# Kernel tuning notes

Measured on AMD Instinct MI355X. Metric: run time of the kernel, lower is better.

## Reference

```python
import jax, jax.numpy as jnp
import numpy as np
import math

CW = 10
T_S = 2.0


def _K(t0):
    t = t0 - CW // 2
    if t < 0:
        return -0.5 * math.exp(t / (T_S / 2.0))
    return math.exp(-t / T_S)

K_VALS = np.array([_K(k) for k in range(CW)], dtype=np.float32)          # synaptic kernel
KS_VALS = np.array([math.exp(-k / T_S) for k in range(CW)], dtype=np.float32)  # spike kernel


def swish(v):
    # original Swish: x * sigmoid(10*x)
    return v * jax.nn.sigmoid(10.0 * v)


def act_fun(v):
    # smooth surrogate spike activation: sigmoid(10*(mem - 0.5)), thresh=0.5
    return jax.nn.sigmoid(10.0 * (v - 0.5))


def setup_inputs() -> dict:
    key = jax.random.key(0)
    k1, k2, k3, k4 = jax.random.split(key, 4)
    B, T = 4096, 50
    x = jax.random.uniform(k1, (B, T, 620), dtype=jnp.float32)
    W1 = jax.random.normal(k2, (200, 620), dtype=jnp.float32) / np.sqrt(620.0)
    W2 = jax.random.normal(k3, (100, 200), dtype=jnp.float32) / np.sqrt(200.0)
    W3 = jax.random.normal(k4, (11, 100), dtype=jnp.float32) / np.sqrt(100.0)
    return {"x": x, "W1": W1, "W2": W2, "W3": W3}


def reference(x, W1, W2, W3):
    B, T, _ = x.shape
    kv = jnp.asarray(K_VALS)
    ks_tail = jnp.asarray(KS_VALS[1:])   # k=1..9; k=0 spike term is always 0 (buffer not yet written)
    kv_tail = jnp.asarray(K_VALS[1:])    # k=1..9 for layer-input history

    # h1 is purely feedforward in time -> precompute, then causal conv with K over CW window.
    h1 = swish(jnp.einsum('btd,nd->btn', x, W1))            # [B, T, 200]
    h1_pad = jnp.pad(h1, ((0, 0), (CW - 1, 0), (0, 0)))
    syn2 = sum(kv[k] * h1_pad[:, CW - 1 - k: CW - 1 - k + T] for k in range(CW))  # [B, T, 200]

    def shift(hist, new):
        # hist[:, j] holds value at time t-1-j; prepend current value
        return jnp.concatenate([new[:, None], hist[:, :-1]], axis=1)

    def step(carry, syn2_t):
        sl2_h, h2_h, sl3_h, h3_h, sl4_h, acc = carry
        # layer 2
        mem2 = syn2_t - jnp.einsum('k,bkn->bn', ks_tail, sl2_h)
        s2 = act_fun(mem2)
        sl2 = s2 * mem2
        h2 = swish(s2 @ W2.T)                                # [B, 100]
        # layer 3
        mem3 = kv[0] * h2 + jnp.einsum('k,bkn->bn', kv_tail, h2_h) \
               - jnp.einsum('k,bkn->bn', ks_tail, sl3_h)
        s3 = act_fun(mem3)
        sl3 = s3 * mem3
        h3 = swish(s3 @ W3.T)                                # [B, 11]
        # layer 4 (output)
        mem4 = kv[0] * h3 + jnp.einsum('k,bkn->bn', kv_tail, h3_h) \
               - jnp.einsum('k,bkn->bn', ks_tail, sl4_h)
        s4 = act_fun(mem4)
        sl4 = s4 * mem4
        carry = (shift(sl2_h, sl2), shift(h2_h, h2), shift(sl3_h, sl3),
                 shift(h3_h, h3), shift(sl4_h, sl4), acc + s4)
        return carry, None

    z = lambda n: jnp.zeros((B, CW - 1, n), dtype=x.dtype)
    carry0 = (z(200), z(100), z(100), z(11), z(11), jnp.zeros((B, 11), dtype=x.dtype))
    carry, _ = jax.lax.scan(step, carry0, jnp.swapaxes(syn2, 0, 1))
    h4_sumspike = carry[-1]
    return h4_sumspike / 50.0
```

## Files before the change

### kernel.cpp

```cpp
#include <hip/hip_runtime.h>
#include <math.h>

#define T_STEPS 50
#define D_IN    620
#define N1      200
#define N2      100
#define N3      11
#define BATCH   4096

typedef short bf16x8 __attribute__((ext_vector_type(8)));
typedef float f32x4  __attribute__((ext_vector_type(4)));

__device__ __constant__ float KV[10] = {
    -0.0033689735f, -0.0091578194f, -0.0248935342f, -0.0676676416f, -0.1839397206f,
     1.0f,           0.6065306597f,  0.3678794412f,  0.2231301601f,  0.1353352832f };

#define RHO    0.60653066f
#define RHO5   0.0820849986f
#define RHO10  0.0067379470f
#define KV0    (-0.0033689735f)
#define C1     (-0.0091578194f)
#define C2     (-0.0248935342f)
#define C3     (-0.0676676416f)
#define C4     (-0.1839397206f)

__device__ __forceinline__ float sigm10(float x) { return 1.0f / (1.0f + __expf(-10.0f * x)); }
__device__ __forceinline__ float swishf(float v) { return v / (1.0f + __expf(-10.0f * v)); }

__device__ __forceinline__ void split2(float x, unsigned short& hi, unsigned short& lo) {
    unsigned u = __float_as_uint(x);
    hi = (unsigned short)(u >> 16);
    float rem = x - __uint_as_float(u & 0xFFFF0000u);
    lo = (unsigned short)(__float_as_uint(rem) >> 16);
}

__global__ void prep_w1(const float* __restrict__ W1, unsigned short* __restrict__ W1pre) {
    int i = blockIdx.x * 256 + threadIdx.x;
    if (i >= 266240) return;
    int kk = i & 31;
    int t1 = i >> 5;
    int n  = t1 % 208;
    int t2 = t1 / 208;
    int p  = t2 & 1;
    int kt = t2 >> 1;
    int k  = kt * 32 + kk;
    float w = (n < N1 && k < D_IN) ? W1[n * D_IN + k] : 0.0f;
    unsigned short hi, lo; split2(w, hi, lo);
    int gsw = (kk >> 3) ^ ((n >> 1) & 3);
    int idx = kt * 13312 + p * 6656 + n * 32 + gsw * 8 + (kk & 7);
    W1pre[idx] = p ? lo : hi;
}

__global__ void prep_w2(const float* __restrict__ W2, unsigned short* __restrict__ W2pre2) {
    int i = blockIdx.x * 256 + threadIdx.x;
    if (i >= 57344) return;
    int e  = i & 7;
    int r  = i >> 3;
    int l  = r & 63;
    int r2 = r >> 6;
    int p  = r2 & 1;
    int r3 = r2 >> 1;
    int ks = r3 % 7;
    int wv = r3 / 7;
    int n  = wv * 16 + (l & 15);
    int k  = ks * 32 + (l >> 4) * 8 + e;
    float v = (n < N2 && k < N1) ? W2[n * N1 + k] : 0.0f;
    unsigned short hi, lo; split2(v, hi, lo);
    W2pre2[i] = p ? lo : hi;
}

__global__ __launch_bounds__(512, 4) void gemm1_mfma(const float* __restrict__ x,
                                                     const unsigned short* __restrict__ W1pre,
                                                     float* __restrict__ h1) {
    __shared__ unsigned short Bs[3][13312];

    const int tid = threadIdx.x;
    const int w   = tid >> 6;
    const int l   = tid & 63;
    const int j   = l >> 4;
    const int r16 = l & 15;
    const long row0 = (long)blockIdx.x * 128;
    const float* arow = x + (row0 + w * 16 + r16) * D_IN;

    f32x4 acc[13];
#pragma unroll
    for (int nt = 0; nt < 13; ++nt) acc[nt] = (f32x4){0.f, 0.f, 0.f, 0.f};

    auto stageB = [&](int kt, int bb) {
        const unsigned short* src = W1pre + kt * 13312;
        unsigned short* dst = &Bs[bb][0];
#pragma unroll
        for (int it = 0; it < 3; ++it) {
            int ch = it * 512 + tid;
            __builtin_amdgcn_global_load_lds(
                (const __attribute__((address_space(1))) unsigned int*)(src + ch * 8),
                (__attribute__((address_space(3))) unsigned int*)(dst + ch * 8), 16, 0, 0);
        }
        if (tid < 128) {
            int ch = 1536 + tid;
            __builtin_amdgcn_global_load_lds(
                (const __attribute__((address_space(1))) unsigned int*)(src + ch * 8),
                (__attribute__((address_space(3))) unsigned int*)(dst + ch * 8), 16, 0, 0);
        }
    };

    auto loadA = [&](int kt, float* av) {
        const float* p = arow + kt * 32 + j * 8;
        const float4 u0 = *(const float4*)p;
        const float4 u1 = *(const float4*)(p + 4);
        av[0] = u0.x; av[1] = u0.y; av[2] = u0.z; av[3] = u0.w;
        av[4] = u1.x; av[5] = u1.y; av[6] = u1.z; av[7] = u1.w;
    };
    auto loadAtail = [&](float* av) {
        if (j == 0) {
            const float4 u0 = *(const float4*)(arow + 608);
            const float4 u1 = *(const float4*)(arow + 612);
            av[0] = u0.x; av[1] = u0.y; av[2] = u0.z; av[3] = u0.w;
            av[4] = u1.x; av[5] = u1.y; av[6] = u1.z; av[7] = u1.w;
        } else if (j == 1) {
            const float4 u0 = *(const float4*)(arow + 616);
            av[0] = u0.x; av[1] = u0.y; av[2] = u0.z; av[3] = u0.w;
            av[4] = 0.f; av[5] = 0.f; av[6] = 0.f; av[7] = 0.f;
        } else {
#pragma unroll
            for (int e = 0; e < 8; ++e) av[e] = 0.f;
        }
    };

    float av[2][8];
    stageB(0, 0);
    stageB(1, 1);
    loadA(0, av[0]);
    loadA(1, av[1]);
    asm volatile("s_waitcnt vmcnt(7)" ::: "memory");
    asm volatile("s_barrier" ::: "memory");

#pragma unroll 1
    for (int kt = 0; kt < 20; ++kt) {
        bf16x8 ah, al;
#pragma unroll
        for (int e = 0; e < 8; ++e) {
            unsigned short hi, lo; split2(av[kt & 1][e], hi, lo);
            ah[e] = (short)hi; al[e] = (short)lo;
        }
        if (kt < 18) {
            if (kt + 2 == 19) loadAtail(av[kt & 1]); else loadA(kt + 2, av[kt & 1]);
            stageB(kt + 2, (kt + 2) % 3);
        }
        const unsigned short* B = &Bs[kt % 3][0];
#pragma unroll
        for (int nt = 0; nt < 13; ++nt) {
            const int n  = nt * 16 + r16;
            const int gs = j ^ ((n >> 1) & 3);
            const bf16x8 bh = *(const bf16x8*)(B + n * 32 + gs * 8);
            const bf16x8 bl = *(const bf16x8*)(B + 6656 + n * 32 + gs * 8);
            acc[nt] = __builtin_amdgcn_mfma_f32_16x16x32_bf16(ah, bh, acc[nt], 0, 0, 0);
            acc[nt] = __builtin_amdgcn_mfma_f32_16x16x32_bf16(ah, bl, acc[nt], 0, 0, 0);
            acc[nt] = __builtin_amdgcn_mfma_f32_16x16x32_bf16(al, bh, acc[nt], 0, 0, 0);
        }
        if (kt < 18) {
            asm volatile("s_waitcnt vmcnt(5)" ::: "memory");
            asm volatile("s_barrier" ::: "memory");
        } else if (kt == 18) {
            asm volatile("s_waitcnt vmcnt(0)" ::: "memory");
            asm volatile("s_barrier" ::: "memory");
        }
    }

#pragma unroll
    for (int nt = 0; nt < 13; ++nt) {
        const int gcol = nt * 16 + r16;
        if (gcol < N1) {
            const long grow0 = row0 + w * 16 + j * 4;
#pragma unroll
            for (int q = 0; q < 4; ++q)
                h1[(grow0 + q) * N1 + gcol] = swishf(acc[nt][q]);
        }
    }
}

__global__ __launch_bounds__(256) void conv_k(float* __restrict__ buf) {
    __shared__ float h1s[T_STEPS * N1];
    const int b = blockIdx.x, tid = threadIdx.x;
    float* p = buf + (size_t)b * (T_STEPS * N1);
    for (int i = tid; i < T_STEPS * N1 / 4; i += 256)
        ((float4*)h1s)[i] = ((const float4*)p)[i];
    __syncthreads();
    for (int i = tid; i < T_STEPS * N1; i += 256) {
        int t = i / N1, n = i - t * N1;
        float s = 0.0f;
#pragma unroll
        for (int k = 0; k < 10; ++k)
            if (k <= t) s = fmaf(KV[k], h1s[(t - k) * N1 + n], s);
        p[i] = s;
    }
}

__global__ __launch_bounds__(512, 2) void snn_scan5(const float* __restrict__ syn2,
                                                    const unsigned short* __restrict__ W2pre2,
                                                    const float* __restrict__ W3,
                                                    float* __restrict__ out) {
    __shared__ __align__(16) unsigned short s2A[8192];
    __shared__ __align__(16) float h2buf[8][132];
    __shared__ __align__(16) float s3buf[8][104];
    __shared__ __align__(16) float W3s[N3 * N2];
    __shared__ __align__(16) float pbuf[8][4][12];

    const int tid = threadIdx.x;
    const int wv  = tid >> 6;
    const int l   = tid & 63;
    const int m16 = l & 15;
    const int j2  = l >> 4;
    const int g   = wv;
    const int c   = l;
    const long b  = (long)blockIdx.x * 8 + g;

    for (int i = tid; i < N3 * N2; i += 512) W3s[i] = W3[i];
    for (int i = tid; i < 8192; i += 512) s2A[i] = 0;

    bf16x8 bh[7], bl[7];
    {
        const unsigned short* wp = W2pre2 + wv * 7168 + l * 8;
#pragma unroll
        for (int ks = 0; ks < 7; ++ks) {
            bh[ks] = *(const bf16x8*)(wp + ks * 1024);
            bl[ks] = *(const bf16x8*)(wp + ks * 1024 + 512);
        }
    }

    const int NL2 = (c < 8)  ? 4 : 3;
    const int NL3 = (c < 36) ? 2 : 1;
    const int o4  = c % 11;
    const int p4  = c / 11;
    const int kbeg = (p4 == 0) ? 0 : (4 + 24 * p4);
    const int nf4  = (p4 == 0) ? 7 : 6;

    float sl2h[10][4] = {}; float Ssl2[4] = {};
    float h2h[10][2]  = {}; float Dd3[2]  = {};
    float sl3h[10][2] = {}; float Ssl3[2] = {};
    float h3h[10]     = {}; float Dd4 = 0.f;
    float sl4h[10]    = {}; float Ssl4 = 0.f;
    float accum       = 0.0f;

    const float* syn2b = syn2 + b * (T_STEPS * N1);
    float syn_nxt[4];
#pragma unroll
    for (int jj = 0; jj < 4; ++jj) syn_nxt[jj] = (jj < NL2) ? syn2b[c + 64 * jj] : 0.0f;

    __syncthreads();

#pragma unroll 1
    for (int tb = 0; tb < T_STEPS; tb += 10) {
#pragma unroll
        for (int u = 0; u < 10; ++u) {
            const int t   = tb + u;
            const int um1 = (u + 9) % 10;
            const int um2 = (u + 8) % 10;
            const int um3 = (u + 7) % 10;
            const int um4 = (u + 6) % 10;
            const int um5 = (u + 5) % 10;

            float syn_cur[4];
#pragma unroll
            for (int jj = 0; jj < 4; ++jj) syn_cur[jj] = syn_nxt[jj];
            if (t + 1 < T_STEPS) {
#pragma unroll
                for (int jj = 0; jj < 4; ++jj)
                    if (jj < NL2) syn_nxt[jj] = syn2b[(t + 1) * N1 + c + 64 * jj];
            }

#pragma unroll
            for (int jj = 0; jj < 4; ++jj) {
                if (jj < NL2) {
                    const int n = c + 64 * jj;
                    const float slp = sl2h[um1][jj];
                    const float slo = sl2h[u][jj];
                    Ssl2[jj] = RHO * (Ssl2[jj] + slp) - RHO10 * slo;
                    const float mem2 = syn_cur[jj] - Ssl2[jj];
                    const float s2   = sigm10(mem2 - 0.5f);
                    sl2h[u][jj] = s2 * mem2;
                    unsigned short hi, lo; split2(s2, hi, lo);
                    const int off = g * 256 + (((n >> 3) ^ (g & 7)) * 8) + (n & 7);
                    s2A[off]        = hi;
                    s2A[4096 + off] = lo;
                }
            }
            __syncthreads();

            {
                f32x4 a0 = (f32x4){0.f, 0.f, 0.f, 0.f};
                f32x4 a1 = (f32x4){0.f, 0.f, 0.f, 0.f};
                const int swz = m16 & 7;
#pragma unroll
                for (int ks = 0; ks < 7; ++ks) {
                    const int gr = (4 * ks + j2) ^ swz;
                    const bf16x8 ahv = *(const bf16x8*)&s2A[m16 * 256 + gr * 8];
                    const bf16x8 alv = *(const bf16x8*)&s2A[4096 + m16 * 256 + gr * 8];
                    if (ks & 1) {
                        a1 = __builtin_amdgcn_mfma_f32_16x16x32_bf16(ahv, bh[ks], a1, 0, 0, 0);
                        a1 = __builtin_amdgcn_mfma_f32_16x16x32_bf16(alv, bh[ks], a1, 0, 0, 0);
                        a1 = __builtin_amdgcn_mfma_f32_16x16x32_bf16(ahv, bl[ks], a1, 0, 0, 0);
                    } else {
                        a0 = __builtin_amdgcn_mfma_f32_16x16x32_bf16(ahv, bh[ks], a0, 0, 0, 0);
                        a0 = __builtin_amdgcn_mfma_f32_16x16x32_bf16(alv, bh[ks], a0, 0, 0, 0);
                        a0 = __builtin_amdgcn_mfma_f32_16x16x32_bf16(ahv, bl[ks], a0, 0, 0, 0);
                    }
                }
                const f32x4 a = a0 + a1;
                if (j2 < 2) {
#pragma unroll
                    for (int q = 0; q < 4; ++q)
                        h2buf[j2 * 4 + q][wv * 16 + m16] = swishf(a[q]);
                }
            }
            __syncthreads();

#pragma unroll
            for (int jj = 0; jj < 2; ++jj) {
                if (jj < NL3) {
                    const int m = c + 64 * jj;
                    const float hm = h2buf[g][m];
                    float gneg = C1 * h2h[um1][jj];
                    gneg = fmaf(C2, h2h[um2][jj], gneg);
                    gneg = fmaf(C3, h2h[um3][jj], gneg);
                    gneg = fmaf(C4, h2h[um4][jj], gneg);
                    Dd3[jj] = fmaf(RHO, Dd3[jj], h2h[um5][jj]);
                    Dd3[jj] = fmaf(-RHO5, h2h[u][jj], Dd3[jj]);
                    const float slp = sl3h[um1][jj];
                    const float slo = sl3h[u][jj];
                    Ssl3[jj] = RHO * (Ssl3[jj] + slp) - RHO10 * slo;
                    const float mem3 = fmaf(KV0, hm, gneg) + Dd3[jj] - Ssl3[jj];
                    const float s3   = sigm10(mem3 - 0.5f);
                    sl3h[u][jj] = s3 * mem3;
                    h2h[u][jj]  = hm;
                    s3buf[g][m] = s3;
                }
            }
            asm volatile("s_waitcnt lgkmcnt(0)" ::: "memory");
            __builtin_amdgcn_sched_barrier(0);

            if (c < 44) {
                float part = 0.0f;
#pragma unroll
                for (int i = 0; i < 7; ++i) {
                    if (i < nf4) {
                        const float4 sv  = *(const float4*)&s3buf[g][kbeg + 4 * i];
                        const float4 wv4 = *(const float4*)&W3s[o4 * N2 + kbeg + 4 * i];
                        part = fmaf(sv.x, wv4.x, part);
                        part = fmaf(sv.y, wv4.y, part);
                        part = fmaf(sv.z, wv4.z, part);
                        part = fmaf(sv.w, wv4.w, part);
                    }
                }
                pbuf[g][p4][o4] = part;
            }
            asm volatile("s_waitcnt lgkmcnt(0)" ::: "memory");
            __builtin_amdgcn_sched_barrier(0);

            if (c < N3) {
                const float a4 = pbuf[g][0][c] + pbuf[g][1][c] + pbuf[g][2][c] + pbuf[g][3][c];
                const float h3 = swishf(a4);
                float gneg = C1 * h3h[um1];
                gneg = fmaf(C2, h3h[um2], gneg);
                gneg = fmaf(C3, h3h[um3], gneg);
                gneg = fmaf(C4, h3h[um4], gneg);
                Dd4 = fmaf(RHO, Dd4, h3h[um5]);
                Dd4 = fmaf(-RHO5, h3h[u], Dd4);
                const float slp = sl4h[um1];
                const float slo = sl4h[u];
                Ssl4 = RHO * (Ssl4 + slp) - RHO10 * slo;
                const float mem4 = fmaf(KV0, h3, gneg) + Dd4 - Ssl4;
                const float s4   = sigm10(mem4 - 0.5f);
                sl4h[u] = s4 * mem4;
                h3h[u]  = h3;
                accum += s4;
            }
        }
    }

    if (c < N3) out[b * N3 + c] = accum * 0.02f;
}

extern "C" void kernel_launch(void* const* d_in, const int* in_sizes, int n_in,
                              void* d_out, int out_size, void* d_ws, size_t ws_size,
                              hipStream_t stream) {
    const float* x  = (const float*)d_in[0];
    const float* W1 = (const float*)d_in[1];
    const float* W2 = (const float*)d_in[2];
    const float* W3 = (const float*)d_in[3];
    float* out = (float*)d_out;

    float* buf = (float*)d_ws;
    unsigned short* W1pre  = (unsigned short*)(buf + (size_t)BATCH * T_STEPS * N1);
    unsigned short* W2pre2 = W1pre + 266240;

    prep_w1<<<1040, 256, 0, stream>>>(W1, W1pre);
    prep_w2<<<224, 256, 0, stream>>>(W2, W2pre2);
    gemm1_mfma<<<1600, 512, 0, stream>>>(x, W1pre, buf);
    conv_k<<<BATCH, 256, 0, stream>>>(buf);
    snn_scan5<<<BATCH / 8, 512, 0, stream>>>(buf, W2pre2, W3, out);
}
```

Measured before the change: 529.7 us.

## Fuse causal conv into scan kernel and double GEMM1 row tile per wave

Removes the separate conv_k kernel by computing the layer-1 synaptic convolution inside the scan, using a 10-entry register history and a decaying recursion like the other layers. This avoids a full read and write pass over the large h1 buffer plus one launch. GEMM1 now gives each wave two 16-row M tiles, so each B fragment loaded from LDS is reused twice. The price is roughly doubled accumulator registers and a lower occupancy bound (2 instead of 4), plus extra register pressure in the scan kernel.

```diff
diff --git a/kernel.cpp b/kernel.cpp
--- a/kernel.cpp
+++ b/kernel.cpp
@@ -10,10 +10,6 @@
 
 typedef short bf16x8 __attribute__((ext_vector_type(8)));
 typedef float f32x4  __attribute__((ext_vector_type(4)));
-
-__device__ __constant__ float KV[10] = {
-    -0.0033689735f, -0.0091578194f, -0.0248935342f, -0.0676676416f, -0.1839397206f,
-     1.0f,           0.6065306597f,  0.3678794412f,  0.2231301601f,  0.1353352832f };
 
 #define RHO    0.60653066f
 #define RHO5   0.0820849986f
@@ -69,7 +65,7 @@
     W2pre2[i] = p ? lo : hi;
 }
 
-__global__ __launch_bounds__(512, 4) void gemm1_mfma(const float* __restrict__ x,
+__global__ __launch_bounds__(512, 2) void gemm1_mfma(const float* __restrict__ x,
                                                      const unsigned short* __restrict__ W1pre,
                                                      float* __restrict__ h1) {
     __shared__ unsigned short Bs[3][13312];
@@ -79,12 +75,14 @@
     const int l   = tid & 63;
     const int j   = l >> 4;
     const int r16 = l & 15;
-    const long row0 = (long)blockIdx.x * 128;
-    const float* arow = x + (row0 + w * 16 + r16) * D_IN;
-
-    f32x4 acc[13];
-#pragma unroll
-    for (int nt = 0; nt < 13; ++nt) acc[nt] = (f32x4){0.f, 0.f, 0.f, 0.f};
+    const long row0 = (long)blockIdx.x * 256;
+    const float* arow0 = x + (row0 + w * 32 + r16) * D_IN;
+
+    f32x4 acc[2][13];
+#pragma unroll
+    for (int mt = 0; mt < 2; ++mt)
+#pragma unroll
+        for (int nt = 0; nt < 13; ++nt) acc[mt][nt] = (f32x4){0.f, 0.f, 0.f, 0.f};
 
     auto stageB = [&](int kt, int bb) {
         const unsigned short* src = W1pre + kt * 13312;
@@ -104,45 +102,54 @@
         }
     };
 
-    auto loadA = [&](int kt, float* av) {
-        const float* p = arow + kt * 32 + j * 8;
-        const float4 u0 = *(const float4*)p;
-        const float4 u1 = *(const float4*)(p + 4);
-        av[0] = u0.x; av[1] = u0.y; av[2] = u0.z; av[3] = u0.w;
-        av[4] = u1.x; av[5] = u1.y; av[6] = u1.z; av[7] = u1.w;
+    auto loadA = [&](int kt, float (&av)[2][8]) {
+#pragma unroll
+        for (int mt = 0; mt < 2; ++mt) {
+            const float* p = arow0 + mt * 16 * D_IN + kt * 32 + j * 8;
+            const float4 u0 = *(const float4*)p;
+            const float4 u1 = *(const float4*)(p + 4);
+            av[mt][0] = u0.x; av[mt][1] = u0.y; av[mt][2] = u0.z; av[mt][3] = u0.w;
+            av[mt][4] = u1.x; av[mt][5] = u1.y; av[mt][6] = u1.z; av[mt][7] = u1.w;
+        }
     };
-    auto loadAtail = [&](float* av) {
-        if (j == 0) {
-            const float4 u0 = *(const float4*)(arow + 608);
-            const float4 u1 = *(const float4*)(arow + 612);
-            av[0] = u0.x; av[1] = u0.y; av[2] = u0.z; av[3] = u0.w;
-            av[4] = u1.x; av[5] = u1.y; av[6] = u1.z; av[7] = u1.w;
-        } else if (j == 1) {
-            const float4 u0 = *(const float4*)(arow + 616);
-            av[0] = u0.x; av[1] = u0.y; av[2] = u0.z; av[3] = u0.w;
-            av[4] = 0.f; av[5] = 0.f; av[6] = 0.f; av[7] = 0.f;
-        } else {
-#pragma unroll
-            for (int e = 0; e < 8; ++e) av[e] = 0.f;
+    auto loadAtail = [&](float (&av)[2][8]) {
+#pragma unroll
+        for (int mt = 0; mt < 2; ++mt) {
+            const float* ar = arow0 + mt * 16 * D_IN;
+            if (j == 0) {
+                const float4 u0 = *(const float4*)(ar + 608);
+                const float4 u1 = *(const float4*)(ar + 612);
+                av[mt][0] = u0.x; av[mt][1] = u0.y; av[mt][2] = u0.z; av[mt][3] = u0.w;
+                av[mt][4] = u1.x; av[mt][5] = u1.y; av[mt][6] = u1.z; av[mt][7] = u1.w;
+            } else if (j == 1) {
+                const float4 u0 = *(const float4*)(ar + 616);
+                av[mt][0] = u0.x; av[mt][1] = u0.y; av[mt][2] = u0.z; av[mt][3] = u0.w;
+                av[mt][4] = 0.f; av[mt][5] = 0.f; av[mt][6] = 0.f; av[mt][7] = 0.f;
+            } else {
+#pragma unroll
+                for (int e = 0; e < 8; ++e) av[mt][e] = 0.f;
+            }
         }
     };
 
-    float av[2][8];
+    float av[2][2][8];
     stageB(0, 0);
     stageB(1, 1);
     loadA(0, av[0]);
     loadA(1, av[1]);
-    asm volatile("s_waitcnt vmcnt(7)" ::: "memory");
+    asm volatile("s_waitcnt vmcnt(11)" ::: "memory");
     asm volatile("s_barrier" ::: "memory");
 
 #pragma unroll 1
     for (int kt = 0; kt < 20; ++kt) {
-        bf16x8 ah, al;
-#pragma unroll
-        for (int e = 0; e < 8; ++e) {
-            unsigned short hi, lo; split2(av[kt & 1][e], hi, lo);
-            ah[e] = (short)hi; al[e] = (short)lo;
-        }
+        bf16x8 ah[2], al[2];
+#pragma unroll
+        for (int mt = 0; mt < 2; ++mt)
+#pragma unroll
+            for (int e = 0; e < 8; ++e) {
+                unsigned short hi, lo; split2(av[kt & 1][mt][e], hi, lo);
+                ah[mt][e] = (short)hi; al[mt][e] = (short)lo;
+            }
         if (kt < 18) {
             if (kt + 2 == 19) loadAtail(av[kt & 1]); else loadA(kt + 2, av[kt & 1]);
             stageB(kt + 2, (kt + 2) % 3);
@@ -154,12 +161,15 @@
             const int gs = j ^ ((n >> 1) & 3);
             const bf16x8 bh = *(const bf16x8*)(B + n * 32 + gs * 8);
             const bf16x8 bl = *(const bf16x8*)(B + 6656 + n * 32 + gs * 8);
-            acc[nt] = __builtin_amdgcn_mfma_f32_16x16x32_bf16(ah, bh, acc[nt], 0, 0, 0);
-            acc[nt] = __builtin_amdgcn_mfma_f32_16x16x32_bf16(ah, bl, acc[nt], 0, 0, 0);
-            acc[nt] = __builtin_amdgcn_mfma_f32_16x16x32_bf16(al, bh, acc[nt], 0, 0, 0);
+            acc[0][nt] = __builtin_amdgcn_mfma_f32_16x16x32_bf16(ah[0], bh, acc[0][nt], 0, 0, 0);
+            acc[1][nt] = __builtin_amdgcn_mfma_f32_16x16x32_bf16(ah[1], bh, acc[1][nt], 0, 0, 0);
+            acc[0][nt] = __builtin_amdgcn_mfma_f32_16x16x32_bf16(ah[0], bl, acc[0][nt], 0, 0, 0);
+            acc[1][nt] = __builtin_amdgcn_mfma_f32_16x16x32_bf16(ah[1], bl, acc[1][nt], 0, 0, 0);
+            acc[0][nt] = __builtin_amdgcn_mfma_f32_16x16x32_bf16(al[0], bh, acc[0][nt], 0, 0, 0);
+            acc[1][nt] = __builtin_amdgcn_mfma_f32_16x16x32_bf16(al[1], bh, acc[1][nt], 0, 0, 0);
         }
         if (kt < 18) {
-            asm volatile("s_waitcnt vmcnt(5)" ::: "memory");
+            asm volatile("s_waitcnt vmcnt(7)" ::: "memory");
             asm volatile("s_barrier" ::: "memory");
         } else if (kt == 18) {
             asm volatile("s_waitcnt vmcnt(0)" ::: "memory");
@@ -168,35 +178,21 @@
     }
 
 #pragma unroll
-    for (int nt = 0; nt < 13; ++nt) {
-        const int gcol = nt * 16 + r16;
-        if (gcol < N1) {
-            const long grow0 = row0 + w * 16 + j * 4;
-#pragma unroll
-            for (int q = 0; q < 4; ++q)
-                h1[(grow0 + q) * N1 + gcol] = swishf(acc[nt][q]);
+    for (int mt = 0; mt < 2; ++mt) {
+        const long grow0 = row0 + w * 32 + mt * 16 + j * 4;
+#pragma unroll
+        for (int nt = 0; nt < 13; ++nt) {
+            const int gcol = nt * 16 + r16;
+            if (gcol < N1) {
+#pragma unroll
+                for (int q = 0; q < 4; ++q)
+                    h1[(grow0 + q) * N1 + gcol] = swishf(acc[mt][nt][q]);
+            }
         }
     }
 }
 
-__global__ __launch_bounds__(256) void conv_k(float* __restrict__ buf) {
-    __shared__ float h1s[T_STEPS * N1];
-    const int b = blockIdx.x, tid = threadIdx.x;
-    float* p = buf + (size_t)b * (T_STEPS * N1);
-    for (int i = tid; i < T_STEPS * N1 / 4; i += 256)
-        ((float4*)h1s)[i] = ((const float4*)p)[i];
-    __syncthreads();
-    for (int i = tid; i < T_STEPS * N1; i += 256) {
-        int t = i / N1, n = i - t * N1;
-        float s = 0.0f;
-#pragma unroll
-        for (int k = 0; k < 10; ++k)
-            if (k <= t) s = fmaf(KV[k], h1s[(t - k) * N1 + n], s);
-        p[i] = s;
-    }
-}
-
-__global__ __launch_bounds__(512, 2) void snn_scan5(const float* __restrict__ syn2,
+__global__ __launch_bounds__(512, 2) void snn_scan6(const float* __restrict__ h1,
                                                     const unsigned short* __restrict__ W2pre2,
                                                     const float* __restrict__ W3,
                                                     float* __restrict__ out) {
@@ -236,16 +232,17 @@
     const int nf4  = (p4 == 0) ? 7 : 6;
 
     float sl2h[10][4] = {}; float Ssl2[4] = {};
+    float h1h[10][4]  = {}; float Dsyn[4] = {};
     float h2h[10][2]  = {}; float Dd3[2]  = {};
     float sl3h[10][2] = {}; float Ssl3[2] = {};
     float h3h[10]     = {}; float Dd4 = 0.f;
     float sl4h[10]    = {}; float Ssl4 = 0.f;
     float accum       = 0.0f;
 
-    const float* syn2b = syn2 + b * (T_STEPS * N1);
-    float syn_nxt[4];
-#pragma unroll
-    for (int jj = 0; jj < 4; ++jj) syn_nxt[jj] = (jj < NL2) ? syn2b[c + 64 * jj] : 0.0f;
+    const float* h1b = h1 + b * (T_STEPS * N1);
+    float h1_nxt[4];
+#pragma unroll
+    for (int jj = 0; jj < 4; ++jj) h1_nxt[jj] = (jj < NL2) ? h1b[c + 64 * jj] : 0.0f;
 
     __syncthreads();
 
@@ -260,25 +257,32 @@
             const int um4 = (u + 6) % 10;
             const int um5 = (u + 5) % 10;
 
-            float syn_cur[4];
-#pragma unroll
-            for (int jj = 0; jj < 4; ++jj) syn_cur[jj] = syn_nxt[jj];
+            float h1_cur[4];
+#pragma unroll
+            for (int jj = 0; jj < 4; ++jj) h1_cur[jj] = h1_nxt[jj];
             if (t + 1 < T_STEPS) {
 #pragma unroll
                 for (int jj = 0; jj < 4; ++jj)
-                    if (jj < NL2) syn_nxt[jj] = syn2b[(t + 1) * N1 + c + 64 * jj];
+                    if (jj < NL2) h1_nxt[jj] = h1b[(t + 1) * N1 + c + 64 * jj];
             }
 
 #pragma unroll
             for (int jj = 0; jj < 4; ++jj) {
                 if (jj < NL2) {
                     const int n = c + 64 * jj;
-                    const float slp = sl2h[um1][jj];
-                    const float slo = sl2h[u][jj];
-                    Ssl2[jj] = RHO * (Ssl2[jj] + slp) - RHO10 * slo;
-                    const float mem2 = syn_cur[jj] - Ssl2[jj];
+                    const float hm1 = h1_cur[jj];
+                    float gneg = C1 * h1h[um1][jj];
+                    gneg = fmaf(C2, h1h[um2][jj], gneg);
+                    gneg = fmaf(C3, h1h[um3][jj], gneg);
+                    gneg = fmaf(C4, h1h[um4][jj], gneg);
+                    Dsyn[jj] = fmaf(RHO, Dsyn[jj], h1h[um5][jj]);
+                    Dsyn[jj] = fmaf(-RHO5, h1h[u][jj], Dsyn[jj]);
+                    const float syn = fmaf(KV0, hm1, gneg) + Dsyn[jj];
+                    Ssl2[jj] = RHO * (Ssl2[jj] + sl2h[um1][jj]) - RHO10 * sl2h[u][jj];
+                    const float mem2 = syn - Ssl2[jj];
                     const float s2   = sigm10(mem2 - 0.5f);
                     sl2h[u][jj] = s2 * mem2;
+                    h1h[u][jj]  = hm1;
                     unsigned short hi, lo; split2(s2, hi, lo);
                     const int off = g * 256 + (((n >> 3) ^ (g & 7)) * 8) + (n & 7);
                     s2A[off]        = hi;
@@ -326,9 +330,7 @@
                     gneg = fmaf(C4, h2h[um4][jj], gneg);
                     Dd3[jj] = fmaf(RHO, Dd3[jj], h2h[um5][jj]);
                     Dd3[jj] = fmaf(-RHO5, h2h[u][jj], Dd3[jj]);
-                    const float slp = sl3h[um1][jj];
-                    const float slo = sl3h[u][jj];
-                    Ssl3[jj] = RHO * (Ssl3[jj] + slp) - RHO10 * slo;
+                    Ssl3[jj] = RHO * (Ssl3[jj] + sl3h[um1][jj]) - RHO10 * sl3h[u][jj];
                     const float mem3 = fmaf(KV0, hm, gneg) + Dd3[jj] - Ssl3[jj];
                     const float s3   = sigm10(mem3 - 0.5f);
                     sl3h[u][jj] = s3 * mem3;
@@ -366,9 +368,7 @@
                 gneg = fmaf(C4, h3h[um4], gneg);
                 Dd4 = fmaf(RHO, Dd4, h3h[um5]);
                 Dd4 = fmaf(-RHO5, h3h[u], Dd4);
-                const float slp = sl4h[um1];
-                const float slo = sl4h[u];
-                Ssl4 = RHO * (Ssl4 + slp) - RHO10 * slo;
+                Ssl4 = RHO * (Ssl4 + sl4h[um1]) - RHO10 * sl4h[u];
                 const float mem4 = fmaf(KV0, h3, gneg) + Dd4 - Ssl4;
                 const float s4   = sigm10(mem4 - 0.5f);
                 sl4h[u] = s4 * mem4;
@@ -396,7 +396,6 @@
 
     prep_w1<<<1040, 256, 0, stream>>>(W1, W1pre);
     prep_w2<<<224, 256, 0, stream>>>(W2, W2pre2);
-    gemm1_mfma<<<1600, 512, 0, stream>>>(x, W1pre, buf);
-    conv_k<<<BATCH, 256, 0, stream>>>(buf);
-    snn_scan5<<<BATCH / 8, 512, 0, stream>>>(buf, W2pre2, W3, out);
-}
+    gemm1_mfma<<<800, 512, 0, stream>>>(x, W1pre, buf);
+    snn_scan6<<<BATCH / 8, 512, 0, stream>>>(buf, W2pre2, W3, out);
+}
```

Measured after the change: 850.8 us. +60.6%, slower.

## Fuse causal conv into scan kernel using register history of h1

Applied to the files above, without the earlier changes.

Removes the separate conv_k kernel and computes the synaptic convolution of h1 inside the scan. It uses a 10-step register ring buffer plus a recursive decay accumulator, the same scheme already used for layers 3 and 4. This saves one full read-modify-write pass over the 4096x50x200 h1 buffer and one kernel launch. In exchange it adds about 40 history registers per thread, and launch bounds drop from 2 to 1 blocks per SM minimum, which may reduce occupancy.

```diff
diff --git a/kernel.cpp b/kernel.cpp
--- a/kernel.cpp
+++ b/kernel.cpp
@@ -10,10 +10,6 @@
 
 typedef short bf16x8 __attribute__((ext_vector_type(8)));
 typedef float f32x4  __attribute__((ext_vector_type(4)));
-
-__device__ __constant__ float KV[10] = {
-    -0.0033689735f, -0.0091578194f, -0.0248935342f, -0.0676676416f, -0.1839397206f,
-     1.0f,           0.6065306597f,  0.3678794412f,  0.2231301601f,  0.1353352832f };
 
 #define RHO    0.60653066f
 #define RHO5   0.0820849986f
@@ -179,24 +175,7 @@
     }
 }
 
-__global__ __launch_bounds__(256) void conv_k(float* __restrict__ buf) {
-    __shared__ float h1s[T_STEPS * N1];
-    const int b = blockIdx.x, tid = threadIdx.x;
-    float* p = buf + (size_t)b * (T_STEPS * N1);
-    for (int i = tid; i < T_STEPS * N1 / 4; i += 256)
-        ((float4*)h1s)[i] = ((const float4*)p)[i];
-    __syncthreads();
-    for (int i = tid; i < T_STEPS * N1; i += 256) {
-        int t = i / N1, n = i - t * N1;
-        float s = 0.0f;
-#pragma unroll
-        for (int k = 0; k < 10; ++k)
-            if (k <= t) s = fmaf(KV[k], h1s[(t - k) * N1 + n], s);
-        p[i] = s;
-    }
-}
-
-__global__ __launch_bounds__(512, 2) void snn_scan5(const float* __restrict__ syn2,
+__global__ __launch_bounds__(512, 1) void snn_scan6(const float* __restrict__ h1,
                                                     const unsigned short* __restrict__ W2pre2,
                                                     const float* __restrict__ W3,
                                                     float* __restrict__ out) {
@@ -236,16 +215,17 @@
     const int nf4  = (p4 == 0) ? 7 : 6;
 
     float sl2h[10][4] = {}; float Ssl2[4] = {};
+    float h1h[10][4]  = {}; float Dsyn[4] = {};
     float h2h[10][2]  = {}; float Dd3[2]  = {};
     float sl3h[10][2] = {}; float Ssl3[2] = {};
     float h3h[10]     = {}; float Dd4 = 0.f;
     float sl4h[10]    = {}; float Ssl4 = 0.f;
     float accum       = 0.0f;
 
-    const float* syn2b = syn2 + b * (T_STEPS * N1);
-    float syn_nxt[4];
-#pragma unroll
-    for (int jj = 0; jj < 4; ++jj) syn_nxt[jj] = (jj < NL2) ? syn2b[c + 64 * jj] : 0.0f;
+    const float* h1b = h1 + b * (T_STEPS * N1);
+    float h1_nxt[4];
+#pragma unroll
+    for (int jj = 0; jj < 4; ++jj) h1_nxt[jj] = (jj < NL2) ? h1b[c + 64 * jj] : 0.0f;
 
     __syncthreads();
 
@@ -260,25 +240,32 @@
             const int um4 = (u + 6) % 10;
             const int um5 = (u + 5) % 10;
 
-            float syn_cur[4];
-#pragma unroll
-            for (int jj = 0; jj < 4; ++jj) syn_cur[jj] = syn_nxt[jj];
+            float h1_cur[4];
+#pragma unroll
+            for (int jj = 0; jj < 4; ++jj) h1_cur[jj] = h1_nxt[jj];
             if (t + 1 < T_STEPS) {
 #pragma unroll
                 for (int jj = 0; jj < 4; ++jj)
-                    if (jj < NL2) syn_nxt[jj] = syn2b[(t + 1) * N1 + c + 64 * jj];
+                    if (jj < NL2) h1_nxt[jj] = h1b[(t + 1) * N1 + c + 64 * jj];
             }
 
 #pragma unroll
             for (int jj = 0; jj < 4; ++jj) {
                 if (jj < NL2) {
                     const int n = c + 64 * jj;
-                    const float slp = sl2h[um1][jj];
-                    const float slo = sl2h[u][jj];
-                    Ssl2[jj] = RHO * (Ssl2[jj] + slp) - RHO10 * slo;
-                    const float mem2 = syn_cur[jj] - Ssl2[jj];
+                    const float hm1 = h1_cur[jj];
+                    float gneg = C1 * h1h[um1][jj];
+                    gneg = fmaf(C2, h1h[um2][jj], gneg);
+                    gneg = fmaf(C3, h1h[um3][jj], gneg);
+                    gneg = fmaf(C4, h1h[um4][jj], gneg);
+                    Dsyn[jj] = fmaf(RHO, Dsyn[jj], h1h[um5][jj]);
+                    Dsyn[jj] = fmaf(-RHO5, h1h[u][jj], Dsyn[jj]);
+                    const float syn = fmaf(KV0, hm1, gneg) + Dsyn[jj];
+                    Ssl2[jj] = RHO * (Ssl2[jj] + sl2h[um1][jj]) - RHO10 * sl2h[u][jj];
+                    const float mem2 = syn - Ssl2[jj];
                     const float s2   = sigm10(mem2 - 0.5f);
                     sl2h[u][jj] = s2 * mem2;
+                    h1h[u][jj]  = hm1;
                     unsigned short hi, lo; split2(s2, hi, lo);
                     const int off = g * 256 + (((n >> 3) ^ (g & 7)) * 8) + (n & 7);
                     s2A[off]        = hi;
@@ -326,9 +313,7 @@
                     gneg = fmaf(C4, h2h[um4][jj], gneg);
                     Dd3[jj] = fmaf(RHO, Dd3[jj], h2h[um5][jj]);
                     Dd3[jj] = fmaf(-RHO5, h2h[u][jj], Dd3[jj]);
-                    const float slp = sl3h[um1][jj];
-                    const float slo = sl3h[u][jj];
-                    Ssl3[jj] = RHO * (Ssl3[jj] + slp) - RHO10 * slo;
+                    Ssl3[jj] = RHO * (Ssl3[jj] + sl3h[um1][jj]) - RHO10 * sl3h[u][jj];
                     const float mem3 = fmaf(KV0, hm, gneg) + Dd3[jj] - Ssl3[jj];
                     const float s3   = sigm10(mem3 - 0.5f);
                     sl3h[u][jj] = s3 * mem3;
@@ -366,9 +351,7 @@
                 gneg = fmaf(C4, h3h[um4], gneg);
                 Dd4 = fmaf(RHO, Dd4, h3h[um5]);
                 Dd4 = fmaf(-RHO5, h3h[u], Dd4);
-                const float slp = sl4h[um1];
-                const float slo = sl4h[u];
-                Ssl4 = RHO * (Ssl4 + slp) - RHO10 * slo;
+                Ssl4 = RHO * (Ssl4 + sl4h[um1]) - RHO10 * sl4h[u];
                 const float mem4 = fmaf(KV0, h3, gneg) + Dd4 - Ssl4;
                 const float s4   = sigm10(mem4 - 0.5f);
                 sl4h[u] = s4 * mem4;
@@ -397,6 +380,5 @@
     prep_w1<<<1040, 256, 0, stream>>>(W1, W1pre);
     prep_w2<<<224, 256, 0, stream>>>(W2, W2pre2);
     gemm1_mfma<<<1600, 512, 0, stream>>>(x, W1pre, buf);
-    conv_k<<<BATCH, 256, 0, stream>>>(buf);
-    snn_scan5<<<BATCH / 8, 512, 0, stream>>>(buf, W2pre2, W3, out);
-}
+    snn_scan6<<<BATCH / 8, 512, 0, stream>>>(buf, W2pre2, W3, out);
+}
```

New measurement: 774.2 us. +46.2%, slower.

## Software-pipeline layer-2 spike computation one timestep ahead in SNN scan

Applied to the files above, without the earlier changes.

Layer 2 depends only on its own history and the precomputed synaptic input, so its membrane update, sigmoid and bf16 hi/lo split for step t+1 are now computed during step t. That work sits after the layer-3 update, where most lanes would otherwise idle while 11 lanes run layer 4. The packed result is held in registers and written to shared memory at the start of the next step, which shortens the serial path before the first barrier of each timestep. The cost is extra live registers for the pending values and one wasted computation past the last step.

```diff
diff --git a/kernel.cpp b/kernel.cpp
--- a/kernel.cpp
+++ b/kernel.cpp
@@ -196,7 +196,29 @@
     }
 }
 
-__global__ __launch_bounds__(512, 2) void snn_scan5(const float* __restrict__ syn2,
+#define P1C(UU, TT)                                                            \
+    {                                                                          \
+        _Pragma("unroll")                                                      \
+        for (int jj = 0; jj < 4; ++jj) {                                       \
+            if (jj < NL2) {                                                    \
+                const float slp = sl2h[((UU) + 9) % 10][jj];                   \
+                const float slo = sl2h[(UU)][jj];                  \
+                Ssl2[jj] = RHO * (Ssl2[jj] + slp) - RHO10 * slo;               \
+                const float mem2 = syn_nxt[jj] - Ssl2[jj];                     \
+                const float s2   = sigm10(mem2 - 0.5f);                        \
+                sl2h[(UU)][jj] = s2 * mem2;                                    \
+                unsigned short hi, lo; split2(s2, hi, lo);                     \
+                pend[jj] = ((unsigned)hi << 16) | (unsigned)lo;                \
+            }                                                                  \
+        }                                                                      \
+        if ((TT) + 1 < T_STEPS) {                                              \
+            _Pragma("unroll")                                                  \
+            for (int jj = 0; jj < 4; ++jj)                                     \
+                if (jj < NL2) syn_nxt[jj] = syn2b[((TT) + 1) * N1 + c + 64 * jj]; \
+        }                                                                      \
+    }
+
+__global__ __launch_bounds__(512, 2) void snn_scan7(const float* __restrict__ syn2,
                                                     const unsigned short* __restrict__ W2pre2,
                                                     const float* __restrict__ W3,
                                                     float* __restrict__ out) {
@@ -241,11 +263,14 @@
     float h3h[10]     = {}; float Dd4 = 0.f;
     float sl4h[10]    = {}; float Ssl4 = 0.f;
     float accum       = 0.0f;
+    unsigned pend[4]  = {0, 0, 0, 0};
 
     const float* syn2b = syn2 + b * (T_STEPS * N1);
     float syn_nxt[4];
 #pragma unroll
     for (int jj = 0; jj < 4; ++jj) syn_nxt[jj] = (jj < NL2) ? syn2b[c + 64 * jj] : 0.0f;
+
+    P1C(0, 0)
 
     __syncthreads();
 
@@ -259,30 +284,15 @@
             const int um3 = (u + 7) % 10;
             const int um4 = (u + 6) % 10;
             const int um5 = (u + 5) % 10;
-
-            float syn_cur[4];
-#pragma unroll
-            for (int jj = 0; jj < 4; ++jj) syn_cur[jj] = syn_nxt[jj];
-            if (t + 1 < T_STEPS) {
-#pragma unroll
-                for (int jj = 0; jj < 4; ++jj)
-                    if (jj < NL2) syn_nxt[jj] = syn2b[(t + 1) * N1 + c + 64 * jj];
-            }
+            const int up1 = (u + 1) % 10;
 
 #pragma unroll
             for (int jj = 0; jj < 4; ++jj) {
                 if (jj < NL2) {
                     const int n = c + 64 * jj;
-                    const float slp = sl2h[um1][jj];
-                    const float slo = sl2h[u][jj];
-                    Ssl2[jj] = RHO * (Ssl2[jj] + slp) - RHO10 * slo;
-                    const float mem2 = syn_cur[jj] - Ssl2[jj];
-                    const float s2   = sigm10(mem2 - 0.5f);
-                    sl2h[u][jj] = s2 * mem2;
-                    unsigned short hi, lo; split2(s2, hi, lo);
                     const int off = g * 256 + (((n >> 3) ^ (g & 7)) * 8) + (n & 7);
-                    s2A[off]        = hi;
-                    s2A[4096 + off] = lo;
+                    s2A[off]        = (unsigned short)(pend[jj] >> 16);
+                    s2A[4096 + off] = (unsigned short)(pend[jj] & 0xFFFFu);
                 }
             }
             __syncthreads();
@@ -326,9 +336,7 @@
                     gneg = fmaf(C4, h2h[um4][jj], gneg);
                     Dd3[jj] = fmaf(RHO, Dd3[jj], h2h[um5][jj]);
                     Dd3[jj] = fmaf(-RHO5, h2h[u][jj], Dd3[jj]);
-                    const float slp = sl3h[um1][jj];
-                    const float slo = sl3h[u][jj];
-                    Ssl3[jj] = RHO * (Ssl3[jj] + slp) - RHO10 * slo;
+                    Ssl3[jj] = RHO * (Ssl3[jj] + sl3h[um1][jj]) - RHO10 * sl3h[u][jj];
                     const float mem3 = fmaf(KV0, hm, gneg) + Dd3[jj] - Ssl3[jj];
                     const float s3   = sigm10(mem3 - 0.5f);
                     sl3h[u][jj] = s3 * mem3;
@@ -336,6 +344,9 @@
                     s3buf[g][m] = s3;
                 }
             }
+
+            P1C(up1, t + 1)
+
             asm volatile("s_waitcnt lgkmcnt(0)" ::: "memory");
             __builtin_amdgcn_sched_barrier(0);
 
@@ -366,9 +377,7 @@
                 gneg = fmaf(C4, h3h[um4], gneg);
                 Dd4 = fmaf(RHO, Dd4, h3h[um5]);
                 Dd4 = fmaf(-RHO5, h3h[u], Dd4);
-                const float slp = sl4h[um1];
-                const float slo = sl4h[u];
-                Ssl4 = RHO * (Ssl4 + slp) - RHO10 * slo;
+                Ssl4 = RHO * (Ssl4 + sl4h[um1]) - RHO10 * sl4h[u];
                 const float mem4 = fmaf(KV0, h3, gneg) + Dd4 - Ssl4;
                 const float s4   = sigm10(mem4 - 0.5f);
                 sl4h[u] = s4 * mem4;
@@ -398,5 +407,5 @@
     prep_w2<<<224, 256, 0, stream>>>(W2, W2pre2);
     gemm1_mfma<<<1600, 512, 0, stream>>>(x, W1pre, buf);
     conv_k<<<BATCH, 256, 0, stream>>>(buf);
-    snn_scan5<<<BATCH / 8, 512, 0, stream>>>(buf, W2pre2, W3, out);
-}
+    snn_scan7<<<BATCH / 8, 512, 0, stream>>>(buf, W2pre2, W3, out);
+}
```

Result: no change. 531.1 us (+0.3%).
